# Kernel tuning notes

Measured on AMD Instinct MI355X. Metric: run time of the kernel, lower is better.

Reference implementation:

```python
import jax, jax.numpy as jnp
import numpy as np

C0 = 32   # number of 0e (scalar) channels
C1 = 16   # number of 1o (vector) channels
NG = 1024 # num_graphs
N = 300000
F = C0 * (C0 + 1) // 2 + C1 * (C1 + 1) // 2  # 664 invariant outputs of TensorSquare->0e


def setup_inputs() -> dict:
    key = jax.random.key(0)
    k1, k2, k3 = jax.random.split(key, 3)
    node_ft = jax.random.normal(k1, (N, C0 + 3 * C1), dtype=jnp.float32)
    batch_index = jnp.sort(jax.random.randint(k2, (N,), 0, NG, dtype=jnp.int32))
    # o3.Linear-style init: normal / sqrt(fan_in)
    W = jax.random.normal(k3, (F, 1), dtype=jnp.float32) / np.float32(np.sqrt(F))
    return {"node_ft": node_ft, "batch_index": batch_index, "num_graphs": NG, "W": W}


def tensor_square_0e(node_ft):
    # Equivariant tensor square keeping only 0e (invariant) outputs:
    #  - symmetric products of scalar channels s_i * s_j (i<=j)
    #  - dot products of vector channels v_i . v_j (i<=j), component-normalized
    s = node_ft[:, :C0]                      # [N, C0]
    v = node_ft[:, C0:].reshape(-1, C1, 3)   # [N, C1, 3]
    i0, j0 = jnp.triu_indices(C0)
    i1, j1 = jnp.triu_indices(C1)
    ts_s = s[:, i0] * s[:, j0]                                  # [N, 528]
    vdot = jnp.einsum('nic,njc->nij', v, v) / jnp.float32(np.sqrt(3.0))
    ts_v = vdot[:, i1, j1]                                      # [N, 136]
    return jnp.concatenate([ts_s, ts_v], axis=1)                # [N, 664]


def reference(node_ft, batch_index, num_graphs, W):
    x = tensor_square_0e(node_ft)            # [N, F]
    x = jax.nn.selu(x)
    x = x @ W                                # [N, 1] attention logits (1x0e)
    ex = jnp.exp(x)                          # [N, 1]
    z = jax.ops.segment_sum(ex, batch_index, num_segments=num_graphs)  # [G, 1]
    attn = ex / z[batch_index]               # segment softmax weights [N, 1]
    out = jax.ops.segment_sum(node_ft * attn, batch_index, num_segments=num_graphs)
    return out                               # [G, C0 + 3*C1]
```

## Files before the change

kernel.cpp:

```cpp
#include <hip/hip_runtime.h>


typedef float f2 __attribute__((ext_vector_type(2)));

#define C0 32
#define C1 16
#define NODE_F 80
#define NG_CONST 1024
#define NPB 320

#define SELU_SCALE 1.0507009873554804934193349852946
#define SELU_ALPHA 1.6732632423543772848170429916717
#define LOG2E      1.4426950408889634073599246810019

#define CS_SCALE 1.2011224087864498f
#define CV_SCALE 0.91271231102878545f

#define WS_S 0
#define WS_Z 81920
#define WS_W 82944

__device__ __forceinline__ int ks_idx(int i, int j) { return i * C0 - (i * (i - 1)) / 2 + (j - i); }
__device__ __forceinline__ int kv_idx(int i, int j) { return 528 + i * C1 - (i * (i - 1)) / 2 + (j - i); }

__global__ __launch_bounds__(256) void prep_kernel(
    const float* __restrict__ W, float* __restrict__ ws)
{
    const int t = blockIdx.x * blockDim.x + threadIdx.x;
    if (t < 82944) {
        ws[t] = 0.0f;
    } else {
        int u = t - 82944;
        if (u < 512) {
            int i = u >> 4, q = u & 15;
            int j0 = 2 * q, j1 = 2 * q + 1;
            ws[WS_W + 2 * u]     = (j0 >= i) ? W[ks_idx(i, j0)] : 0.0f;
            ws[WS_W + 2 * u + 1] = (j1 >= i) ? W[ks_idx(i, j1)] : 0.0f;
        } else if (u < 640) {
            int v = u - 512;
            int i = v >> 3, q = v & 7;
            int j0 = 2 * q, j1 = 2 * q + 1;
            ws[WS_W + 1024 + 2 * v]     = (j0 >= i) ? W[kv_idx(i, j0)] : 0.0f;
            ws[WS_W + 1024 + 2 * v + 1] = (j1 >= i) ? W[kv_idx(i, j1)] : 0.0f;
        }
    }
}

__global__ __launch_bounds__(NPB, 2) void main_kernel(
    const float* __restrict__ nf, const int* __restrict__ bi,
    const float* __restrict__ ws, float* __restrict__ S,
    float* __restrict__ z, int N)
{
    __shared__ __align__(16) float Wlds[1280];
    __shared__ float exl[NPB];
    __shared__ int   bil[NPB];

    const int tid  = threadIdx.x;
    const int base = blockIdx.x * NPB;
    const float4* g4 = (const float4*)nf;

    #pragma unroll
    for (int u = tid; u < 1280; u += NPB) Wlds[u] = ws[WS_W + u];

    const int  n     = base + tid;
    const bool valid = (n < N);
    const int  nn    = valid ? n : (N - 1);
    bil[tid] = bi[nn];
    __syncthreads();

    float4 row4[20];
    #pragma unroll
    for (int q = 0; q < 20; ++q) row4[q] = g4[(size_t)nn * 20 + q];
    const float* row = (const float*)row4;

    const f2* WsL = (const f2*)Wlds;
    const f2* WvL = (const f2*)(Wlds + 1024);

    f2 accA[2], accB[2];
    accA[0] = (f2)0.f; accA[1] = (f2)0.f; accB[0] = (f2)0.f; accB[1] = (f2)0.f;

    {
        f2 s2[C0 / 2];
        #pragma unroll
        for (int q = 0; q < C0 / 2; ++q)
            s2[q] = f2{row[2 * q], row[2 * q + 1]} * CS_SCALE;
        #pragma unroll
        for (int i = 0; i < C0; ++i) {
            const float si = (i & 1) ? s2[i >> 1].y : s2[i >> 1].x;
            const f2 si2 = f2{si, si};
            #pragma unroll
            for (int q = i >> 1; q < C0 / 2; ++q) {
                f2 f = si2 * s2[q];
                f2 p = __builtin_elementwise_max(f, (f2)0.f);
                f2 m = __builtin_elementwise_min(f, (f2)0.f);
                f2 e; e.x = __builtin_amdgcn_exp2f(m.x);
                      e.y = __builtin_amdgcn_exp2f(m.y);
                f2 w = WsL[i * 16 + q];
                accA[q & 1] = __builtin_elementwise_fma(w, p, accA[q & 1]);
                accB[q & 1] = __builtin_elementwise_fma(w, e, accB[q & 1]);
            }
        }
    }
    {
        f2 vp[C1 / 2][3];
        #pragma unroll
        for (int q = 0; q < C1 / 2; ++q) {
            #pragma unroll
            for (int c = 0; c < 3; ++c)
                vp[q][c] = f2{row[C0 + 6 * q + c], row[C0 + 6 * q + 3 + c]} * CV_SCALE;
        }
        #pragma unroll
        for (int i = 0; i < C1; ++i) {
            const int iq = i >> 1;
            const float vi0 = (i & 1) ? vp[iq][0].y : vp[iq][0].x;
            const float vi1 = (i & 1) ? vp[iq][1].y : vp[iq][1].x;
            const float vi2 = (i & 1) ? vp[iq][2].y : vp[iq][2].x;
            #pragma unroll
            for (int q = i >> 1; q < C1 / 2; ++q) {
                f2 f = vp[q][0] * f2{vi0, vi0};
                f = __builtin_elementwise_fma(vp[q][1], f2{vi1, vi1}, f);
                f = __builtin_elementwise_fma(vp[q][2], f2{vi2, vi2}, f);
                f2 p = __builtin_elementwise_max(f, (f2)0.f);
                f2 m = __builtin_elementwise_min(f, (f2)0.f);
                f2 e; e.x = __builtin_amdgcn_exp2f(m.x);
                      e.y = __builtin_amdgcn_exp2f(m.y);
                f2 w = WvL[i * 8 + q];
                accA[q & 1] = __builtin_elementwise_fma(w, p, accA[q & 1]);
                accB[q & 1] = __builtin_elementwise_fma(w, e, accB[q & 1]);
            }
        }
    }

    const float A1 = accA[0].x + accA[0].y + accA[1].x + accA[1].y;
    const float A2 = accB[0].x + accB[0].y + accB[1].x + accB[1].y;
    const float l2 = fmaf((float)SELU_SCALE, A1,
                          (float)(SELU_SCALE * SELU_ALPHA * LOG2E) * A2);
    exl[tid] = valid ? __builtin_amdgcn_exp2f(l2) : 0.0f;
    __syncthreads();

    const int no = tid / 20;
    const int c4 = tid % 20;
    int cg = bil[no * 20];
    float4 acc = make_float4(0.f, 0.f, 0.f, 0.f);
    float  zacc = 0.0f;

    #pragma unroll
    for (int k = 0; k < 20; ++k) {
        const int nl = no * 20 + k;
        const int g2 = bil[nl];
        if (g2 != cg) {
            unsafeAtomicAdd(&S[cg * NODE_F + c4 * 4 + 0], acc.x);
            unsafeAtomicAdd(&S[cg * NODE_F + c4 * 4 + 1], acc.y);
            unsafeAtomicAdd(&S[cg * NODE_F + c4 * 4 + 2], acc.z);
            unsafeAtomicAdd(&S[cg * NODE_F + c4 * 4 + 3], acc.w);
            if (c4 == 0) unsafeAtomicAdd(&z[cg], zacc);
            acc = make_float4(0.f, 0.f, 0.f, 0.f); zacc = 0.0f; cg = g2;
        }
        int idx = base + nl; if (idx > N - 1) idx = N - 1;
        const float  w = exl[nl];
        const float4 v = g4[(size_t)idx * 20 + c4];
        acc.x = fmaf(v.x, w, acc.x); acc.y = fmaf(v.y, w, acc.y);
        acc.z = fmaf(v.z, w, acc.z); acc.w = fmaf(v.w, w, acc.w);
        zacc += w;
    }
    unsafeAtomicAdd(&S[cg * NODE_F + c4 * 4 + 0], acc.x);
    unsafeAtomicAdd(&S[cg * NODE_F + c4 * 4 + 1], acc.y);
    unsafeAtomicAdd(&S[cg * NODE_F + c4 * 4 + 2], acc.z);
    unsafeAtomicAdd(&S[cg * NODE_F + c4 * 4 + 3], acc.w);
    if (c4 == 0) unsafeAtomicAdd(&z[cg], zacc);
}

__global__ __launch_bounds__(256) void divide_kernel(
    const float* __restrict__ S, const float* __restrict__ z,
    float* __restrict__ out)
{
    const int t = blockIdx.x * blockDim.x + threadIdx.x;
    if (t >= NG_CONST * NODE_F) return;
    const float zz = z[t / NODE_F];
    out[t] = (zz > 0.0f) ? (S[t] / zz) : 0.0f;
}

extern "C" void kernel_launch(void* const* d_in, const int* in_sizes, int n_in,
                              void* d_out, int out_size, void* d_ws, size_t ws_size,
                              hipStream_t stream) {
    const float* nf = (const float*)d_in[0];
    const int*   bi = (const int*)d_in[1];
    const float* W  = (const float*)d_in[3];
    float* out = (float*)d_out;

    const int N = in_sizes[0] / NODE_F;
    float* ws = (float*)d_ws;
    float* S  = ws + WS_S;
    float* z  = ws + WS_Z;

    hipLaunchKernelGGL(prep_kernel, dim3(332), dim3(256), 0, stream, W, ws);
    hipLaunchKernelGGL(main_kernel, dim3((N + NPB - 1) / NPB), dim3(NPB), 0, stream,
                       nf, bi, ws, S, z, N);
    hipLaunchKernelGGL(divide_kernel, dim3((NG_CONST * NODE_F + 255) / 256), dim3(256),
                       0, stream, S, z, out);
}
```

Before: 195.2 us.

## Process two nodes per thread with packed f2 math and uniform scalar weights

```diff
diff --git a/kernel.cpp b/kernel.cpp
--- a/kernel.cpp
+++ b/kernel.cpp
@@ -8,6 +8,7 @@
 #define NODE_F 80
 #define NG_CONST 1024
 #define NPB 320
+#define NODES_PB 640
 
 #define SELU_SCALE 1.0507009873554804934193349852946
 #define SELU_ALPHA 1.6732632423543772848170429916717
@@ -18,135 +19,112 @@
 
 #define WS_S 0
 #define WS_Z 81920
-#define WS_W 82944
 
-__device__ __forceinline__ int ks_idx(int i, int j) { return i * C0 - (i * (i - 1)) / 2 + (j - i); }
-__device__ __forceinline__ int kv_idx(int i, int j) { return 528 + i * C1 - (i * (i - 1)) / 2 + (j - i); }
-
-__global__ __launch_bounds__(256) void prep_kernel(
-    const float* __restrict__ W, float* __restrict__ ws)
+__global__ __launch_bounds__(256) void prep_kernel(float* __restrict__ ws)
 {
     const int t = blockIdx.x * blockDim.x + threadIdx.x;
-    if (t < 82944) {
-        ws[t] = 0.0f;
-    } else {
-        int u = t - 82944;
-        if (u < 512) {
-            int i = u >> 4, q = u & 15;
-            int j0 = 2 * q, j1 = 2 * q + 1;
-            ws[WS_W + 2 * u]     = (j0 >= i) ? W[ks_idx(i, j0)] : 0.0f;
-            ws[WS_W + 2 * u + 1] = (j1 >= i) ? W[ks_idx(i, j1)] : 0.0f;
-        } else if (u < 640) {
-            int v = u - 512;
-            int i = v >> 3, q = v & 7;
-            int j0 = 2 * q, j1 = 2 * q + 1;
-            ws[WS_W + 1024 + 2 * v]     = (j0 >= i) ? W[kv_idx(i, j0)] : 0.0f;
-            ws[WS_W + 1024 + 2 * v + 1] = (j1 >= i) ? W[kv_idx(i, j1)] : 0.0f;
-        }
-    }
+    if (t < 82944) ws[t] = 0.0f;
 }
 
-__global__ __launch_bounds__(NPB, 2) void main_kernel(
+__global__ __launch_bounds__(NPB)
+__attribute__((amdgpu_waves_per_eu(2, 3)))
+void main_kernel(
     const float* __restrict__ nf, const int* __restrict__ bi,
-    const float* __restrict__ ws, float* __restrict__ S,
+    const float* __restrict__ W, float* __restrict__ S,
     float* __restrict__ z, int N)
 {
-    __shared__ __align__(16) float Wlds[1280];
-    __shared__ float exl[NPB];
-    __shared__ int   bil[NPB];
+    __shared__ float exl[NODES_PB];
+    __shared__ int   bil[NODES_PB];
 
     const int tid  = threadIdx.x;
-    const int base = blockIdx.x * NPB;
+    const int base = blockIdx.x * NODES_PB;
     const float4* g4 = (const float4*)nf;
 
-    #pragma unroll
-    for (int u = tid; u < 1280; u += NPB) Wlds[u] = ws[WS_W + u];
+    const int  na = base + tid;
+    const int  nb = na + NPB;
+    const bool va = (na < N), vb = (nb < N);
+    const int  ea = va ? na : (N - 1);
+    const int  eb = vb ? nb : (N - 1);
+    bil[tid]       = bi[ea];
+    bil[tid + NPB] = bi[eb];
 
-    const int  n     = base + tid;
-    const bool valid = (n < N);
-    const int  nn    = valid ? n : (N - 1);
-    bil[tid] = bi[nn];
-    __syncthreads();
-
-    float4 row4[20];
-    #pragma unroll
-    for (int q = 0; q < 20; ++q) row4[q] = g4[(size_t)nn * 20 + q];
-    const float* row = (const float*)row4;
-
-    const f2* WsL = (const f2*)Wlds;
-    const f2* WvL = (const f2*)(Wlds + 1024);
+    const float4* rpa = g4 + (size_t)ea * 20;
+    const float4* rpb = g4 + (size_t)eb * 20;
 
     f2 accA[2], accB[2];
     accA[0] = (f2)0.f; accA[1] = (f2)0.f; accB[0] = (f2)0.f; accB[1] = (f2)0.f;
+    int k = 0;
 
     {
-        f2 s2[C0 / 2];
+        f2 s2[C0];
         #pragma unroll
-        for (int q = 0; q < C0 / 2; ++q)
-            s2[q] = f2{row[2 * q], row[2 * q + 1]} * CS_SCALE;
+        for (int q = 0; q < 8; ++q) {
+            float4 A = rpa[q], B = rpb[q];
+            s2[4 * q + 0] = f2{A.x, B.x} * CS_SCALE;
+            s2[4 * q + 1] = f2{A.y, B.y} * CS_SCALE;
+            s2[4 * q + 2] = f2{A.z, B.z} * CS_SCALE;
+            s2[4 * q + 3] = f2{A.w, B.w} * CS_SCALE;
+        }
         #pragma unroll
         for (int i = 0; i < C0; ++i) {
-            const float si = (i & 1) ? s2[i >> 1].y : s2[i >> 1].x;
-            const f2 si2 = f2{si, si};
             #pragma unroll
-            for (int q = i >> 1; q < C0 / 2; ++q) {
-                f2 f = si2 * s2[q];
+            for (int j = i; j < C0; ++j) {
+                f2 f = s2[i] * s2[j];
                 f2 p = __builtin_elementwise_max(f, (f2)0.f);
                 f2 m = __builtin_elementwise_min(f, (f2)0.f);
                 f2 e; e.x = __builtin_amdgcn_exp2f(m.x);
                       e.y = __builtin_amdgcn_exp2f(m.y);
-                f2 w = WsL[i * 16 + q];
-                accA[q & 1] = __builtin_elementwise_fma(w, p, accA[q & 1]);
-                accB[q & 1] = __builtin_elementwise_fma(w, e, accB[q & 1]);
+                const float w = W[k]; ++k;
+                accA[j & 1] = __builtin_elementwise_fma((f2)w, p, accA[j & 1]);
+                accB[j & 1] = __builtin_elementwise_fma((f2)w, e, accB[j & 1]);
             }
         }
     }
     {
-        f2 vp[C1 / 2][3];
+        f2 vs2[3 * C1];
         #pragma unroll
-        for (int q = 0; q < C1 / 2; ++q) {
-            #pragma unroll
-            for (int c = 0; c < 3; ++c)
-                vp[q][c] = f2{row[C0 + 6 * q + c], row[C0 + 6 * q + 3 + c]} * CV_SCALE;
+        for (int q = 0; q < 12; ++q) {
+            float4 A = rpa[8 + q], B = rpb[8 + q];
+            vs2[4 * q + 0] = f2{A.x, B.x} * CV_SCALE;
+            vs2[4 * q + 1] = f2{A.y, B.y} * CV_SCALE;
+            vs2[4 * q + 2] = f2{A.z, B.z} * CV_SCALE;
+            vs2[4 * q + 3] = f2{A.w, B.w} * CV_SCALE;
         }
         #pragma unroll
         for (int i = 0; i < C1; ++i) {
-            const int iq = i >> 1;
-            const float vi0 = (i & 1) ? vp[iq][0].y : vp[iq][0].x;
-            const float vi1 = (i & 1) ? vp[iq][1].y : vp[iq][1].x;
-            const float vi2 = (i & 1) ? vp[iq][2].y : vp[iq][2].x;
             #pragma unroll
-            for (int q = i >> 1; q < C1 / 2; ++q) {
-                f2 f = vp[q][0] * f2{vi0, vi0};
-                f = __builtin_elementwise_fma(vp[q][1], f2{vi1, vi1}, f);
-                f = __builtin_elementwise_fma(vp[q][2], f2{vi2, vi2}, f);
+            for (int j = i; j < C1; ++j) {
+                f2 f = vs2[3 * i] * vs2[3 * j];
+                f = __builtin_elementwise_fma(vs2[3 * i + 1], vs2[3 * j + 1], f);
+                f = __builtin_elementwise_fma(vs2[3 * i + 2], vs2[3 * j + 2], f);
                 f2 p = __builtin_elementwise_max(f, (f2)0.f);
                 f2 m = __builtin_elementwise_min(f, (f2)0.f);
                 f2 e; e.x = __builtin_amdgcn_exp2f(m.x);
                       e.y = __builtin_amdgcn_exp2f(m.y);
-                f2 w = WvL[i * 8 + q];
-                accA[q & 1] = __builtin_elementwise_fma(w, p, accA[q & 1]);
-                accB[q & 1] = __builtin_elementwise_fma(w, e, accB[q & 1]);
+                const float w = W[k]; ++k;
+                accA[j & 1] = __builtin_elementwise_fma((f2)w, p, accA[j & 1]);
+                accB[j & 1] = __builtin_elementwise_fma((f2)w, e, accB[j & 1]);
             }
         }
     }
 
-    const float A1 = accA[0].x + accA[0].y + accA[1].x + accA[1].y;
-    const float A2 = accB[0].x + accB[0].y + accB[1].x + accB[1].y;
-    const float l2 = fmaf((float)SELU_SCALE, A1,
-                          (float)(SELU_SCALE * SELU_ALPHA * LOG2E) * A2);
-    exl[tid] = valid ? __builtin_amdgcn_exp2f(l2) : 0.0f;
+    f2 A1 = accA[0] + accA[1];
+    f2 A2 = accB[0] + accB[1];
+    f2 l2 = A1 * (float)SELU_SCALE;
+    l2 = __builtin_elementwise_fma((f2)(float)(SELU_SCALE * SELU_ALPHA * LOG2E), A2, l2);
+    exl[tid]       = va ? __builtin_amdgcn_exp2f(l2.x) : 0.0f;
+    exl[tid + NPB] = vb ? __builtin_amdgcn_exp2f(l2.y) : 0.0f;
     __syncthreads();
 
     const int no = tid / 20;
     const int c4 = tid % 20;
-    int cg = bil[no * 20];
+    int cg = bil[no * 40];
     float4 acc = make_float4(0.f, 0.f, 0.f, 0.f);
     float  zacc = 0.0f;
 
-    #pragma unroll
-    for (int k = 0; k < 20; ++k) {
-        const int nl = no * 20 + k;
+    #pragma unroll 4
+    for (int kk = 0; kk < 40; ++kk) {
+        const int nl = no * 40 + kk;
         const int g2 = bil[nl];
         if (g2 != cg) {
             unsafeAtomicAdd(&S[cg * NODE_F + c4 * 4 + 0], acc.x);
@@ -193,9 +171,9 @@
     float* S  = ws + WS_S;
     float* z  = ws + WS_Z;
 
-    hipLaunchKernelGGL(prep_kernel, dim3(332), dim3(256), 0, stream, W, ws);
-    hipLaunchKernelGGL(main_kernel, dim3((N + NPB - 1) / NPB), dim3(NPB), 0, stream,
-                       nf, bi, ws, S, z, N);
+    hipLaunchKernelGGL(prep_kernel, dim3(324), dim3(256), 0, stream, ws);
+    hipLaunchKernelGGL(main_kernel, dim3((N + NODES_PB - 1) / NODES_PB), dim3(NPB),
+                       0, stream, nf, bi, W, S, z, N);
     hipLaunchKernelGGL(divide_kernel, dim3((NG_CONST * NODE_F + 255) / 256), dim3(256),
                        0, stream, S, z, out);
 }
```

Result: slower. 226.8 us (+16.2%).

## Read weights via uniform scalar global loads and stream row blocks instead of staging

Applied to the files above, without the earlier changes.

```diff
diff --git a/kernel.cpp b/kernel.cpp
--- a/kernel.cpp
+++ b/kernel.cpp
@@ -12,13 +12,15 @@
 #define SELU_SCALE 1.0507009873554804934193349852946
 #define SELU_ALPHA 1.6732632423543772848170429916717
 #define LOG2E      1.4426950408889634073599246810019
-
-#define CS_SCALE 1.2011224087864498f
-#define CV_SCALE 0.91271231102878545f
-
-#define WS_S 0
-#define WS_Z 81920
-#define WS_W 82944
+#define SQRT3      1.7320508075688772935274463415059
+
+#define CS2 ((float)LOG2E)
+#define CV2 ((float)(LOG2E / SQRT3))
+
+#define WS_S   0
+#define WS_Z   81920
+#define WS_WST 82944
+#define WS_WVT 83968
 
 __device__ __forceinline__ int ks_idx(int i, int j) { return i * C0 - (i * (i - 1)) / 2 + (j - i); }
 __device__ __forceinline__ int kv_idx(int i, int j) { return 528 + i * C1 - (i * (i - 1)) / 2 + (j - i); }
@@ -29,104 +31,127 @@
     const int t = blockIdx.x * blockDim.x + threadIdx.x;
     if (t < 82944) {
         ws[t] = 0.0f;
-    } else {
+    } else if (t < 82944 + 512) {
         int u = t - 82944;
-        if (u < 512) {
-            int i = u >> 4, q = u & 15;
-            int j0 = 2 * q, j1 = 2 * q + 1;
-            ws[WS_W + 2 * u]     = (j0 >= i) ? W[ks_idx(i, j0)] : 0.0f;
-            ws[WS_W + 2 * u + 1] = (j1 >= i) ? W[ks_idx(i, j1)] : 0.0f;
-        } else if (u < 640) {
-            int v = u - 512;
-            int i = v >> 3, q = v & 7;
-            int j0 = 2 * q, j1 = 2 * q + 1;
-            ws[WS_W + 1024 + 2 * v]     = (j0 >= i) ? W[kv_idx(i, j0)] : 0.0f;
-            ws[WS_W + 1024 + 2 * v + 1] = (j1 >= i) ? W[kv_idx(i, j1)] : 0.0f;
-        }
-    }
-}
-
-__global__ __launch_bounds__(NPB, 2) void main_kernel(
+        int q = u >> 5, i = u & 31;
+        int j0 = 2 * q, j1 = 2 * q + 1;
+        ws[WS_WST + 2 * u]     = (j0 >= i) ? W[ks_idx(i, j0)] : 0.0f;
+        ws[WS_WST + 2 * u + 1] = (j1 >= i) ? W[ks_idx(i, j1)] : 0.0f;
+    } else if (t < 82944 + 512 + 128) {
+        int u = t - 82944 - 512;
+        int q = u >> 4, i = u & 15;
+        int j0 = 2 * q, j1 = 2 * q + 1;
+        ws[WS_WVT + 2 * u]     = (j0 >= i) ? W[kv_idx(i, j0)] : 0.0f;
+        ws[WS_WVT + 2 * u + 1] = (j1 >= i) ? W[kv_idx(i, j1)] : 0.0f;
+    }
+}
+
+__global__ __launch_bounds__(NPB) void main_kernel(
     const float* __restrict__ nf, const int* __restrict__ bi,
     const float* __restrict__ ws, float* __restrict__ S,
     float* __restrict__ z, int N)
 {
-    __shared__ __align__(16) float Wlds[1280];
     __shared__ float exl[NPB];
     __shared__ int   bil[NPB];
 
     const int tid  = threadIdx.x;
     const int base = blockIdx.x * NPB;
     const float4* g4 = (const float4*)nf;
-
-    #pragma unroll
-    for (int u = tid; u < 1280; u += NPB) Wlds[u] = ws[WS_W + u];
+    const f2* Wst = (const f2*)(ws + WS_WST);
+    const f2* Wvt = (const f2*)(ws + WS_WVT);
 
     const int  n     = base + tid;
     const bool valid = (n < N);
     const int  nn    = valid ? n : (N - 1);
     bil[tid] = bi[nn];
-    __syncthreads();
-
-    float4 row4[20];
-    #pragma unroll
-    for (int q = 0; q < 20; ++q) row4[q] = g4[(size_t)nn * 20 + q];
-    const float* row = (const float*)row4;
-
-    const f2* WsL = (const f2*)Wlds;
-    const f2* WvL = (const f2*)(Wlds + 1024);
+
+    const float4* rp = g4 + (size_t)nn * 20;
 
     f2 accA[2], accB[2];
     accA[0] = (f2)0.f; accA[1] = (f2)0.f; accB[0] = (f2)0.f; accB[1] = (f2)0.f;
 
-    {
-        f2 s2[C0 / 2];
+    #pragma unroll
+    for (int ib = 0; ib < 4; ++ib) {
+        float4 a0 = rp[2 * ib], a1 = rp[2 * ib + 1];
+        float su[8];
+        su[0] = a0.x * CS2; su[1] = a0.y * CS2; su[2] = a0.z * CS2; su[3] = a0.w * CS2;
+        su[4] = a1.x * CS2; su[5] = a1.y * CS2; su[6] = a1.z * CS2; su[7] = a1.w * CS2;
+
         #pragma unroll
-        for (int q = 0; q < C0 / 2; ++q)
-            s2[q] = f2{row[2 * q], row[2 * q + 1]} * CS_SCALE;
-        #pragma unroll
-        for (int i = 0; i < C0; ++i) {
-            const float si = (i & 1) ? s2[i >> 1].y : s2[i >> 1].x;
-            const f2 si2 = f2{si, si};
+        for (int qq = 4 * ib; qq < 16; qq += 2) {
+            float4 v = rp[qq >> 1];
+            f2 sj0 = f2{v.x, v.y};
+            f2 sj1 = f2{v.z, v.w};
             #pragma unroll
-            for (int q = i >> 1; q < C0 / 2; ++q) {
-                f2 f = si2 * s2[q];
-                f2 p = __builtin_elementwise_max(f, (f2)0.f);
-                f2 m = __builtin_elementwise_min(f, (f2)0.f);
-                f2 e; e.x = __builtin_amdgcn_exp2f(m.x);
-                      e.y = __builtin_amdgcn_exp2f(m.y);
-                f2 w = WsL[i * 16 + q];
-                accA[q & 1] = __builtin_elementwise_fma(w, p, accA[q & 1]);
-                accB[q & 1] = __builtin_elementwise_fma(w, e, accB[q & 1]);
+            for (int u = 0; u < 8; ++u) {
+                const int i = 8 * ib + u;
+                {
+                    f2 f = sj0 * (f2)su[u];
+                    f2 p = __builtin_elementwise_max(f, (f2)0.f);
+                    f2 m = __builtin_elementwise_min(f, (f2)0.f);
+                    f2 e; e.x = __builtin_amdgcn_exp2f(m.x);
+                          e.y = __builtin_amdgcn_exp2f(m.y);
+                    f2 w = Wst[qq * 32 + i];
+                    accA[0] = __builtin_elementwise_fma(w, p, accA[0]);
+                    accB[0] = __builtin_elementwise_fma(w, e, accB[0]);
+                }
+                {
+                    f2 f = sj1 * (f2)su[u];
+                    f2 p = __builtin_elementwise_max(f, (f2)0.f);
+                    f2 m = __builtin_elementwise_min(f, (f2)0.f);
+                    f2 e; e.x = __builtin_amdgcn_exp2f(m.x);
+                          e.y = __builtin_amdgcn_exp2f(m.y);
+                    f2 w = Wst[(qq + 1) * 32 + i];
+                    accA[1] = __builtin_elementwise_fma(w, p, accA[1]);
+                    accB[1] = __builtin_elementwise_fma(w, e, accB[1]);
+                }
             }
         }
     }
-    {
-        f2 vp[C1 / 2][3];
+
+    #pragma unroll
+    for (int ib = 0; ib < 4; ++ib) {
+        float4 b0 = rp[8 + 3 * ib], b1 = rp[9 + 3 * ib], b2 = rp[10 + 3 * ib];
+        float vi[4][3];
+        vi[0][0] = b0.x * CV2; vi[0][1] = b0.y * CV2; vi[0][2] = b0.z * CV2;
+        vi[1][0] = b0.w * CV2; vi[1][1] = b1.x * CV2; vi[1][2] = b1.y * CV2;
+        vi[2][0] = b1.z * CV2; vi[2][1] = b1.w * CV2; vi[2][2] = b2.x * CV2;
+        vi[3][0] = b2.y * CV2; vi[3][1] = b2.z * CV2; vi[3][2] = b2.w * CV2;
+
         #pragma unroll
-        for (int q = 0; q < C1 / 2; ++q) {
+        for (int qq = 2 * ib; qq < 8; qq += 2) {
+            const int jb = 8 + 3 * (qq >> 1);
+            float4 A = rp[jb], B = rp[jb + 1], C = rp[jb + 2];
+            const float ax = A.x, ay = A.y, az = A.z;
+            const float bx = A.w, by = B.x, bz = B.y;
+            const float cx = B.z, cy = B.w, cz = C.x;
+            const float dx = C.y, dy = C.z, dz = C.w;
             #pragma unroll
-            for (int c = 0; c < 3; ++c)
-                vp[q][c] = f2{row[C0 + 6 * q + c], row[C0 + 6 * q + 3 + c]} * CV_SCALE;
-        }
-        #pragma unroll
-        for (int i = 0; i < C1; ++i) {
-            const int iq = i >> 1;
-            const float vi0 = (i & 1) ? vp[iq][0].y : vp[iq][0].x;
-            const float vi1 = (i & 1) ? vp[iq][1].y : vp[iq][1].x;
-            const float vi2 = (i & 1) ? vp[iq][2].y : vp[iq][2].x;
-            #pragma unroll
-            for (int q = i >> 1; q < C1 / 2; ++q) {
-                f2 f = vp[q][0] * f2{vi0, vi0};
-                f = __builtin_elementwise_fma(vp[q][1], f2{vi1, vi1}, f);
-                f = __builtin_elementwise_fma(vp[q][2], f2{vi2, vi2}, f);
-                f2 p = __builtin_elementwise_max(f, (f2)0.f);
-                f2 m = __builtin_elementwise_min(f, (f2)0.f);
-                f2 e; e.x = __builtin_amdgcn_exp2f(m.x);
-                      e.y = __builtin_amdgcn_exp2f(m.y);
-                f2 w = WvL[i * 8 + q];
-                accA[q & 1] = __builtin_elementwise_fma(w, p, accA[q & 1]);
-                accB[q & 1] = __builtin_elementwise_fma(w, e, accB[q & 1]);
+            for (int u = 0; u < 4; ++u) {
+                const int i = 4 * ib + u;
+                const float x = vi[u][0], y = vi[u][1], zc = vi[u][2];
+                {
+                    f2 f = f2{fmaf(x, ax, fmaf(y, ay, zc * az)),
+                              fmaf(x, bx, fmaf(y, by, zc * bz))};
+                    f2 p = __builtin_elementwise_max(f, (f2)0.f);
+                    f2 m = __builtin_elementwise_min(f, (f2)0.f);
+                    f2 e; e.x = __builtin_amdgcn_exp2f(m.x);
+                          e.y = __builtin_amdgcn_exp2f(m.y);
+                    f2 w = Wvt[qq * 16 + i];
+                    accA[0] = __builtin_elementwise_fma(w, p, accA[0]);
+                    accB[0] = __builtin_elementwise_fma(w, e, accB[0]);
+                }
+                {
+                    f2 f = f2{fmaf(x, cx, fmaf(y, cy, zc * cz)),
+                              fmaf(x, dx, fmaf(y, dy, zc * dz))};
+                    f2 p = __builtin_elementwise_max(f, (f2)0.f);
+                    f2 m = __builtin_elementwise_min(f, (f2)0.f);
+                    f2 e; e.x = __builtin_amdgcn_exp2f(m.x);
+                          e.y = __builtin_amdgcn_exp2f(m.y);
+                    f2 w = Wvt[(qq + 1) * 16 + i];
+                    accA[1] = __builtin_elementwise_fma(w, p, accA[1]);
+                    accB[1] = __builtin_elementwise_fma(w, e, accB[1]);
+                }
             }
         }
     }
@@ -193,9 +218,9 @@
     float* S  = ws + WS_S;
     float* z  = ws + WS_Z;
 
-    hipLaunchKernelGGL(prep_kernel, dim3(332), dim3(256), 0, stream, W, ws);
-    hipLaunchKernelGGL(main_kernel, dim3((N + NPB - 1) / NPB), dim3(NPB), 0, stream,
-                       nf, bi, ws, S, z, N);
+    hipLaunchKernelGGL(prep_kernel, dim3(330), dim3(256), 0, stream, W, ws);
+    hipLaunchKernelGGL(main_kernel, dim3((N + NPB - 1) / NPB), dim3(NPB),
+                       0, stream, nf, bi, ws, S, z, N);
     hipLaunchKernelGGL(divide_kernel, dim3((NG_CONST * NODE_F + 255) / 256), dim3(256),
                        0, stream, S, z, out);
 }
```

Measured after the change: 232.0 us. 18.9% more time.
